# Kernel tuning notes

Measured on AMD Instinct MI355X. Metric: run time of the kernel, lower is better.

Reference implementation:

```python
import jax, jax.numpy as jnp
import numpy as np

D_MODEL = 1024
D_HEAD = 64
RANK = 8
LEAF = 4
NUM_LEAVES = D_HEAD // LEAF            # 16
NUM_LEVELS = 4                          # log2(64/4)
BLOCK_SIZES = [4, 8, 16, 32]
RANKS = [min(RANK, b) for b in BLOCK_SIZES]   # [4,8,8,8]
NUM_NODES = [NUM_LEAVES // 2 ** (l + 1) for l in range(NUM_LEVELS)]  # [8,4,2,1]


def _elu1(x):
    return jax.nn.elu(x) + 1.0


def setup_inputs() -> dict:
    key = jax.random.key(0)
    ks = jax.random.split(key, 32)
    B, T = 8, 2048
    x = jax.random.normal(ks[0], (B, T, D_MODEL), jnp.float32)
    s_in = 1.0 / np.sqrt(D_MODEL)
    s_out = 1.0 / np.sqrt(D_HEAD)
    inp = {
        'x': x,
        'Wq': jax.random.normal(ks[1], (D_MODEL, D_HEAD), jnp.float32) * s_in,
        'Wk': jax.random.normal(ks[2], (D_MODEL, D_HEAD), jnp.float32) * s_in,
        'Wv': jax.random.normal(ks[3], (D_MODEL, D_HEAD), jnp.float32) * s_in,
        'Wo': jax.random.normal(ks[4], (D_HEAD, D_MODEL), jnp.float32) * s_out,
    }
    # Fixed orthonormal bases per level (torch.linalg.qr of randn in original)
    idx = 5
    for name in ['UL', 'VR', 'UR', 'VL']:
        for l in range(NUM_LEVELS):
            bs, rl = BLOCK_SIZES[l], RANKS[l]
            Q, _ = jnp.linalg.qr(jax.random.normal(ks[idx], (bs, rl), jnp.float32))
            inp[f'{name}{l}'] = Q
            idx += 1
    return inp


def _hss_forward(x, Wq, Wk, Wv, Wo, UL, VR, UR, VL):
    B, T, _ = x.shape
    q = _elu1(x @ Wq)   # (B,T,Dh)
    k = _elu1(x @ Wk)
    v = x @ Wv

    leaf0 = jnp.zeros((B, NUM_LEAVES, LEAF, LEAF), x.dtype)
    Ws0 = tuple(jnp.zeros((B, NUM_NODES[l], RANKS[l], RANKS[l]), x.dtype)
                for l in range(NUM_LEVELS))
    z0 = jnp.zeros((B, D_HEAD), x.dtype)

    def step(carry, kvq):
        leaf, Ws, z = carry
        k_t, v_t, q_t = kvq  # each (B, Dh)
        # rank-1 update: leaf diagonal blocks
        leaf = leaf + jnp.einsum('bni,bnj->bnij',
                                 k_t.reshape(B, NUM_LEAVES, LEAF),
                                 v_t.reshape(B, NUM_LEAVES, LEAF))
        newWs = []
        for l in range(NUM_LEVELS):
            bs, nn = BLOCK_SIZES[l], NUM_NODES[l]
            u_r = k_t.reshape(B, nn, 2 * bs)
            v_r = v_t.reshape(B, nn, 2 * bs)
            uL = jnp.einsum('bnd,dr->bnr', u_r[:, :, :bs], UL[l])
            vR = jnp.einsum('bnd,dr->bnr', v_r[:, :, bs:], VR[l])
            newWs.append(Ws[l] + jnp.einsum('bni,bnj->bnij', uL, vR))
        Ws = tuple(newWs)
        z = z + k_t
        # HSS matvec: y = S @ q_t
        y = jnp.einsum('bnij,bnj->bni', leaf,
                       q_t.reshape(B, NUM_LEAVES, LEAF)).reshape(B, D_HEAD)
        for l in range(NUM_LEVELS):
            bs, nn = BLOCK_SIZES[l], NUM_NODES[l]
            x_r = q_t.reshape(B, nn, 2 * bs)
            vr_x = jnp.einsum('bnd,dr->bnr', x_r[:, :, bs:], VR[l])
            y_top = jnp.einsum('dr,bnr->bnd', UL[l],
                               jnp.einsum('bnij,bnj->bni', Ws[l], vr_x))
            vl_x = jnp.einsum('bnd,dr->bnr', x_r[:, :, :bs], VL[l])
            y_bot = jnp.einsum('dr,bnr->bnd', UR[l],
                               jnp.einsum('bnji,bnj->bni', Ws[l], vl_x))
            y = y + jnp.concatenate([y_top, y_bot], axis=-1).reshape(B, D_HEAD)
        denom = jnp.maximum(jnp.sum(z * q_t, axis=-1, keepdims=True), 1e-6)
        return (leaf, Ws, z), y / denom

    kvq = (jnp.swapaxes(k, 0, 1), jnp.swapaxes(v, 0, 1), jnp.swapaxes(q, 0, 1))
    _, outs = jax.lax.scan(step, (leaf0, Ws0, z0), kvq)  # (T,B,Dh)
    out = jnp.swapaxes(outs, 0, 1)  # (B,T,Dh); dropout is identity in eval
    return out @ Wo


def reference(x, Wq, Wk, Wv, Wo,
              UL0, UL1, UL2, UL3,
              VR0, VR1, VR2, VR3,
              UR0, UR1, UR2, UR3,
              VL0, VL1, VL2, VL3):
    UL = (UL0, UL1, UL2, UL3)
    VR = (VR0, VR1, VR2, VR3)
    UR = (UR0, UR1, UR2, UR3)
    VL = (VL0, VL1, VL2, VL3)
    return _hss_forward(x, Wq, Wk, Wv, Wo, UL, VR, UR, VL)
```

## Files before the change

### kernel.cpp

```cpp
#include <hip/hip_runtime.h>
#include <hip/hip_bf16.h>

typedef unsigned short u16;
typedef __attribute__((ext_vector_type(8))) short bf16x8;
typedef __attribute__((ext_vector_type(4))) float f32x4;

#define B_ 8
#define T_ 2048
#define BT_ (B_*T_)
#define DM_ 1024
#define DH_ 64
#define NCH_ 128
#define S_ (T_/NCH_)
#define STATE_ 896
#define UVP 180

__device__ __forceinline__ float b2f(u16 u){ unsigned v=((unsigned)u)<<16; float f; __builtin_memcpy(&f,&v,4); return f; }
__device__ __forceinline__ u16 f2b(float f){ __hip_bfloat16 h=__float2bfloat16(f); u16 u; __builtin_memcpy(&u,&h,2); return u; }

__device__ __forceinline__ float ldin(const void* p, size_t i, int f32){
  return f32 ? ((const float*)p)[i] : b2f(((const u16*)p)[i]);
}
__device__ __forceinline__ bf16x8 ld8bf(const void* p, size_t i, int f32){
  if (f32){
    f32x4 v0 = *(const f32x4*)((const float*)p + i);
    f32x4 v1 = *(const f32x4*)((const float*)p + i + 4);
    bf16x8 r;
    #pragma unroll
    for (int j=0;j<4;j++){ r[j] = (short)f2b(v0[j]); r[4+j] = (short)f2b(v1[j]); }
    return r;
  }
  return *(const bf16x8*)((const u16*)p + i);
}

__device__ __forceinline__ void gl_lds16(const void* g, void* l){
  __builtin_amdgcn_global_load_lds((const __attribute__((address_space(1))) unsigned int*)g,
                                   (__attribute__((address_space(3))) unsigned int*)l, 16, 0, 0);
}

__device__ __forceinline__ void decodeWs(int e, int& ia, int& ib){
  if (e<384){ int o=e-256, n=o>>4; ia=n*4+((o>>2)&3); ib=n*4+(o&3); }
  else if (e<640){ int o=e-384, n=o>>6; ia=32+n*8+((o>>3)&7); ib=32+n*8+(o&7); }
  else if (e<768){ int o=e-640, n=o>>6; ia=64+n*8+((o>>3)&7); ib=64+n*8+(o&7); }
  else { int o=e-768; ia=80+((o>>3)&7); ib=80+(o&7); }
}
__device__ __forceinline__ void decode88(int f, int& l, int& n, int& ri){
  if (f<32){ l=0; n=f>>2; ri=f&3; }
  else if (f<64){ l=1; n=(f-32)>>3; ri=f&7; }
  else if (f<80){ l=2; n=(f-64)>>3; ri=f&7; }
  else { l=3; n=0; ri=f&7; }
}

__global__ __launch_bounds__(64) void k_detect(const u16* __restrict__ x, int* __restrict__ flag){
  int tid = threadIdx.x;
  int sane = 0;
  for (int i = tid; i < 4096; i += 64){
    u16 u = x[i];
    int e = (u >> 7) & 0xFF;
    if ((u & 0x7FFF) == 0 || (e >= 100 && e <= 140)) sane++;
  }
  #pragma unroll
  for (int o = 32; o > 0; o >>= 1) sane += __shfl_down(sane, o);
  if (tid == 0) flag[0] = (sane < 3600) ? 1 : 0;
}

__global__ __launch_bounds__(256) void k_wfrag(
    const void* __restrict__ Wq, const void* __restrict__ Wk, const void* __restrict__ Wv,
    const void* __restrict__ Wo,
    const void* __restrict__ UL0, const void* __restrict__ UL1, const void* __restrict__ UL2, const void* __restrict__ UL3,
    const void* __restrict__ VR0, const void* __restrict__ VR1, const void* __restrict__ VR2, const void* __restrict__ VR3,
    const void* __restrict__ VL0, const void* __restrict__ VL1, const void* __restrict__ VL2, const void* __restrict__ VL3,
    u16* __restrict__ WF, u16* __restrict__ WoF, u16* __restrict__ PF,
    const int* __restrict__ fl)
{
  const int f32 = fl[0];
  int e = blockIdx.x*256 + threadIdx.x;
  if (e < 24576){
    int m = e >> 13;
    int rem = e & 8191;
    int ks = rem >> 8;
    int nt = (rem >> 6) & 3;
    int lane = rem & 63;
    const void* W = (m==0)?Wq:((m==1)?Wk:Wv);
    int kr = ks*32 + (lane>>4)*8;
    int col = nt*16 + (lane&15);
    u16 o[8];
    #pragma unroll
    for (int j=0;j<8;j++) o[j] = f2b(ldin(W, (size_t)(kr+j)*DH_ + col, f32));
    u16* dst = WF + (size_t)e*8;
    #pragma unroll
    for (int j=0;j<8;j++) dst[j] = o[j];
  } else if (e < 32768){
    int eo = e - 24576;
    int ks = eo >> 12;
    int nt = (eo >> 6) & 63;
    int lane = eo & 63;
    int kr = ks*32 + (lane>>4)*8;
    int col = nt*16 + (lane&15);
    u16 o[8];
    #pragma unroll
    for (int j=0;j<8;j++) o[j] = f2b(ldin(Wo, (size_t)(kr+j)*DM_ + col, f32));
    u16* dst = WoF + (size_t)eo*8;
    #pragma unroll
    for (int j=0;j<8;j++) dst[j] = o[j];
  } else if (e < 35072){
    int pe = e - 32768;
    int lane = pe & 63;
    int nt = (pe >> 6) % 6;
    int mk = pe / 384;
    int ks = mk & 1, mat = mk >> 1;
    int col = nt*16 + (lane&15);
    int dbase = ks*32 + (lane>>4)*8;
    const int BSl[4]={4,8,16,32}; const int Rl[4]={4,8,8,8};
    u16 o[8];
    #pragma unroll
    for (int j=0;j<8;j++){
      float val = 0.f;
      if (col < 88){
        int l,n,ri; decode88(col,l,n,ri);
        int bs=BSl[l], r=Rl[l];
        int lo = n*2*bs + ((mat==1)?bs:0);
        int d = dbase + j;
        if (d >= lo && d < lo+bs){
          const void* Up;
          if (mat==0)      Up = (l==0)?UL0:(l==1)?UL1:(l==2)?UL2:UL3;
          else if (mat==1) Up = (l==0)?VR0:(l==1)?VR1:(l==2)?VR2:VR3;
          else             Up = (l==0)?VL0:(l==1)?VL1:(l==2)?VL2:VL3;
          val = ldin(Up, (size_t)(d-lo)*r + ri, f32);
        }
      }
      o[j] = f2b(val);
    }
    u16* dst = PF + (size_t)pe*8;
    #pragma unroll
    for (int j=0;j<8;j++) dst[j] = o[j];
  }
}

__global__ __launch_bounds__(512, 4) void k_proj7(
    const void* __restrict__ x, const u16* __restrict__ WF,
    float* __restrict__ oq, float* __restrict__ ok_, float* __restrict__ ov,
    u16* __restrict__ qb16, u16* __restrict__ kb16, u16* __restrict__ vb16,
    const int* __restrict__ fl)
{
  __shared__ __align__(16) char sh[49152];
  const int f32 = fl[0];
  const int tid = threadIdx.x;
  const int wv = tid>>6;
  const int mg = wv>>1;
  const int h  = wv&1;
  const int lane = tid&63;
  const int quad = lane>>4, l16 = lane&15;
  const int rows0 = blockIdx.x*64 + mg*16;
  const size_t rowA = (size_t)(rows0 + l16)*DM_;

  f32x4 acc[12];
  #pragma unroll
  for (int i=0;i<12;i++) acc[i] = (f32x4){0.f,0.f,0.f,0.f};

  #define STAGE(t, buf) do{                                                   \
    _Pragma("unroll")                                                         \
    for (int r=0;r<3;r++){                                                    \
      int s = wv + r*8;                                                       \
      int hs = (s>=12) ? 1 : 0;                                               \
      int f = s - hs*12;                                                      \
      int m_ = f>>2, nt_ = f&3;                                               \
      int ks_ = hs*16 + (t);                                                  \
      const char* src = (const char*)WF + (size_t)((m_*32+ks_)*4+nt_)*1024 + (size_t)lane*16; \
      char* dst = sh + (buf)*24576 + hs*12288 + f*1024 + lane*16;             \
      gl_lds16(src, dst);                                                     \
    } }while(0)

  STAGE(0, 0);
  bf16x8 a_cur = ld8bf(x, rowA + (size_t)(h*16)*32 + quad*8, f32);
  asm volatile("s_waitcnt vmcnt(0)" ::: "memory");
  __syncthreads();

  bf16x8 a_nxt = a_cur;
  for (int t=0;t<16;t++){
    int buf = t&1;
    if (t<15){
      STAGE(t+1, buf^1);
      a_nxt = ld8bf(x, rowA + (size_t)(h*16+t+1)*32 + quad*8, f32);
    }
    const char* bb = sh + buf*24576 + h*12288;
    #pragma unroll
    for (int f=0;f<12;f++){
      bf16x8 b = *(const bf16x8*)(bb + f*1024 + lane*16);
      acc[f] = __builtin_amdgcn_mfma_f32_16x16x32_bf16(a_cur, b, acc[f],0,0,0);
    }
    a_cur = a_nxt;
    asm volatile("s_waitcnt vmcnt(0)" ::: "memory");
    __syncthreads();
  }
  #undef STAGE

  if (h==1){
    #pragma unroll
    for (int i=0;i<12;i++) ((f32x4*)sh)[(mg*12+i)*64 + lane] = acc[i];
  }
  __syncthreads();
  if (h==0){
    #pragma unroll
    for (int i=0;i<12;i++){
      f32x4 r = ((f32x4*)sh)[(mg*12+i)*64 + lane];
      acc[i][0]+=r[0]; acc[i][1]+=r[1]; acc[i][2]+=r[2]; acc[i][3]+=r[3];
    }
    #pragma unroll
    for (int m=0;m<3;m++){
      float* __restrict__ outp = (m==0)?oq:((m==1)?ok_:ov);
      u16* __restrict__ outb = (m==0)?qb16:((m==1)?kb16:vb16);
      #pragma unroll
      for (int nt=0;nt<4;nt++){
        #pragma unroll
        for (int i=0;i<4;i++){
          int row = rows0 + quad*4 + i;
          int col = nt*16 + l16;
          float val = acc[m*4+nt][i];
          if (m<2) val = (val>0.f)? (val+1.f) : expf(val);
          outp[(size_t)row*DH_ + col] = val;
          outb[(size_t)row*DH_ + col] = f2b(val);
        }
      }
    }
  }
}

__global__ __launch_bounds__(64) void k_prep3(
    const u16* __restrict__ qb16, const u16* __restrict__ kb16, const u16* __restrict__ vb16,
    const u16* __restrict__ PF,
    float* __restrict__ uLa, float* __restrict__ vRa, float* __restrict__ vrxa, float* __restrict__ vlxa)
{
  const int m = blockIdx.y;
  const int rows0 = blockIdx.x*16;
  const int lane = threadIdx.x;
  const int quad = lane>>4, l16 = lane&15;

  const u16* __restrict__ src = (m==0)?kb16:((m==1)?vb16:qb16);
  const int mat = (m==0)?0:((m==3)?2:1);

  bf16x8 a[2];
  #pragma unroll
  for (int ks=0;ks<2;ks++){
    size_t off = (size_t)(rows0 + l16)*DH_ + ks*32 + quad*8;
    a[ks] = *(const bf16x8*)(src + off);
  }
  f32x4 acc[6];
  #pragma unroll
  for (int nt=0;nt<6;nt++) acc[nt] = (f32x4){0.f,0.f,0.f,0.f};

  #pragma unroll
  for (int ks=0;ks<2;ks++){
    #pragma unroll
    for (int nt=0;nt<6;nt++){
      bf16x8 b = *(const bf16x8*)(PF + ((size_t)((mat*2+ks)*6+nt)*64 + lane)*8);
      acc[nt] = __builtin_amdgcn_mfma_f32_16x16x32_bf16(a[ks], b, acc[nt],0,0,0);
    }
  }
  float* __restrict__ dst = (m==0)?uLa:(m==1)?vRa:(m==2)?vrxa:vlxa;
  #pragma unroll
  for (int nt=0;nt<6;nt++){
    int col = nt*16 + l16;
    if (col < 88){
      #pragma unroll
      for (int i=0;i<4;i++){
        int row = rows0 + quad*4 + i;
        dst[(size_t)row*88 + col] = acc[nt][i];
      }
    }
  }
}

__global__ __launch_bounds__(256) void k_chunksum(
    const float* __restrict__ gk, const float* __restrict__ gv,
    const float* __restrict__ uLa, const float* __restrict__ vRa,
    float* __restrict__ SL)
{
  const int bid = blockIdx.x;
  const int b = bid/NCH_, c = bid%NCH_;
  const size_t base64 = (size_t)(b*T_ + c*S_)*64;
  const size_t base88 = (size_t)(b*T_ + c*S_)*88;
  for (int p=0;p<4;p++){
    int e = threadIdx.x + p*256;
    if (e>=STATE_) break;
    float acc=0.f;
    if (e < 256){
      int n=e>>4;
      const float* A = gk + base64 + n*4 + ((e>>2)&3);
      const float* Bp = gv + base64 + n*4 + (e&3);
      for (int s=0;s<S_;s++) acc += A[s*64]*Bp[s*64];
    } else if (e < 832){
      int ia, ib; decodeWs(e, ia, ib);
      const float* A = uLa + base88 + ia;
      const float* Bp = vRa + base88 + ib;
      for (int s=0;s<S_;s++) acc += A[s*88]*Bp[s*88];
    } else {
      const float* A = gk + base64 + (e-832);
      for (int s=0;s<S_;s++) acc += A[s*64];
    }
    SL[(size_t)bid*STATE_ + e] = acc;
  }
}

__global__ __launch_bounds__(224) void k_prefix(const float* __restrict__ SL, float* __restrict__ SP){
  const int b = blockIdx.x;
  int e = blockIdx.y*224 + threadIdx.x;
  if (e >= STATE_) return;
  float run=0.f;
  for (int c=0;c<NCH_;c++){
    size_t idx = ((size_t)(b*NCH_+c))*STATE_ + e;
    SP[idx] = run; run += SL[idx];
  }
}

__global__ __launch_bounds__(128) void k_intra(
    const float* __restrict__ gq, const float* __restrict__ gk, const float* __restrict__ gv,
    const float* __restrict__ uLa, const float* __restrict__ vRa,
    const float* __restrict__ vrxa, const float* __restrict__ vlxa,
    const float* __restrict__ SP,
    const void* __restrict__ UL0, const void* __restrict__ UL1, const void* __restrict__ UL2, const void* __restrict__ UL3,
    const void* __restrict__ UR0, const void* __restrict__ UR1, const void* __restrict__ UR2, const void* __restrict__ UR3,
    u16* __restrict__ Yb, const int* __restrict__ fl)
{
  __shared__ float kS[S_*64];
  __shared__ float vS[S_*64];
  __shared__ float uvS[S_*UVP];
  __shared__ float st0[STATE_];
  __shared__ float ULs[520], URs[520];
  const int f32 = fl[0];
  const int tid = threadIdx.x;
  const int bid = blockIdx.x;
  const int b = bid/NCH_, c = bid%NCH_;
  const int row0 = b*T_ + c*S_;

  const size_t r64 = (size_t)row0*64;
  for (int i=tid;i<S_*64;i+=128){ kS[i]=gk[r64+i]; vS[i]=gv[r64+i]; }
  const size_t r88 = (size_t)row0*88;
  for (int i=tid;i<S_*88;i+=128){
    int s=i/88, f=i-s*88;
    uvS[s*UVP+f]    = uLa[r88+i];
    uvS[s*UVP+88+f] = vRa[r88+i];
  }
  for (int e=tid;e<STATE_;e+=128) st0[e] = SP[(size_t)bid*STATE_+e];
  for (int e=tid;e<464;e+=128){
    int l, idx;
    if (e<16){ l=0; idx=e; } else if (e<80){ l=1; idx=e-16; }
    else if (e<208){ l=2; idx=e-80; } else { l=3; idx=e-208; }
    const void* ul = (l==0)?UL0:(l==1)?UL1:(l==2)?UL2:UL3;
    const void* ur = (l==0)?UR0:(l==1)?UR1:(l==2)?UR2:UR3;
    int dst = (l==0) ? e :
              (l==1) ? 16  + (idx>>3)*9 + (idx&7) :
              (l==2) ? 88  + (idx>>3)*9 + (idx&7) :
                       232 + (idx>>3)*9 + (idx&7);
    ULs[dst] = ldin(ul, idx, f32); URs[dst] = ldin(ur, idx, f32);
  }
  __syncthreads();

  const int w = tid>>6, lane = tid&63, tl = lane>>3, g = lane&7;
  const int t = w*8 + tl;
  const int n1 = g>>1, ri1 = (g&1)*4;
  const int n2 = g>>2, ri2 = (g&3)*2;
  const size_t row = (size_t)(row0 + t);

  float qr[8];
  { const float* qp = gq + row*64 + g*8;
    *(f32x4*)&qr[0] = *(const f32x4*)qp; *(f32x4*)&qr[4] = *(const f32x4*)(qp+4); }
  float rxL0[4], lxL0[4], rxL1[8], lxL1[8], rxL2[8], lxL2[8], rxL3[8], lxL3[8];
  { const float* rp = vrxa + row*88; const float* lp = vlxa + row*88;
    *(f32x4*)&rxL0[0] = *(const f32x4*)(rp + 4*g);
    *(f32x4*)&lxL0[0] = *(const f32x4*)(lp + 4*g);
    *(f32x4*)&rxL1[0] = *(const f32x4*)(rp + 32 + n1*8); *(f32x4*)&rxL1[4] = *(const f32x4*)(rp + 36 + n1*8);
    *(f32x4*)&lxL1[0] = *(const f32x4*)(lp + 32 + n1*8); *(f32x4*)&lxL1[4] = *(const f32x4*)(lp + 36 + n1*8);
    *(f32x4*)&rxL2[0] = *(const f32x4*)(rp + 64 + n2*8); *(f32x4*)&rxL2[4] = *(const f32x4*)(rp + 68 + n2*8);
    *(f32x4*)&lxL2[0] = *(const f32x4*)(lp + 64 + n2*8); *(f32x4*)&lxL2[4] = *(const f32x4*)(lp + 68 + n2*8);
    *(f32x4*)&rxL3[0] = *(const f32x4*)(rp + 80); *(f32x4*)&rxL3[4] = *(const f32x4*)(rp + 84);
    *(f32x4*)&lxL3[0] = *(const f32x4*)(lp + 80); *(f32x4*)&lxL3[4] = *(const f32x4*)(lp + 84); }

  float yacc[8], den = 0.f;
  #pragma unroll
  for (int cc=0;cc<8;cc++){
    int n = 2*g + (cc>>2);
    const float* m = &st0[n*16 + (cc&3)*4];
    const float* qp = &qr[(cc>>2)*4];
    yacc[cc] = m[0]*qp[0]+m[1]*qp[1]+m[2]*qp[2]+m[3]*qp[3];
    den += st0[832 + g*8 + cc]*qr[cc];
  }
  float gtL0[4], gbL0[4], gtL1[4], gbL1[4], gtL2[2], gbL2[2], gtL3, gbL3;
  #pragma unroll
  for (int cc=0;cc<4;cc++){
    const float* m = &st0[256 + g*16 + cc*4];
    gtL0[cc] = m[0]*rxL0[0]+m[1]*rxL0[1]+m[2]*rxL0[2]+m[3]*rxL0[3];
    float s2 = 0.f;
    #pragma unroll
    for (int j=0;j<4;j++) s2 += st0[256 + g*16 + j*4 + cc]*lxL0[j];
    gbL0[cc] = s2;
  }
  #pragma unroll
  for (int cc=0;cc<4;cc++){
    int ri = ri1 + cc;
    float s1=0.f, s2=0.f;
    #pragma unroll
    for (int j=0;j<8;j++){
      s1 += st0[384 + n1*64 + ri*8 + j]*rxL1[j];
      s2 += st0[384 + n1*64 + j*8 + ri]*lxL1[j];
    }
    gtL1[cc]=s1; gbL1[cc]=s2;
  }
  #pragma unroll
  for (int cc=0;cc<2;cc++){
    int ri = ri2 + cc;
    float s1=0.f, s2=0.f;
    #pragma unroll
    for (int j=0;j<8;j++){
      s1 += st0[640 + n2*64 + ri*8 + j]*rxL2[j];
      s2 += st0[640 + n2*64 + j*8 + ri]*lxL2[j];
    }
    gtL2[cc]=s1; gbL2[cc]=s2;
  }
  { float s1=0.f, s2=0.f;
    #pragma unroll
    for (int j=0;j<8;j++){
      s1 += st0[768 + g*8 + j]*rxL3[j];
      s2 += st0[768 + j*8 + g]*lxL3[j];
    }
    gtL3=s1; gbL3=s2; }

  const int smax = w*8 + 8;
  for (int s=0; s<smax; s++){
    const float* ks_ = &kS[s*64 + g*8];
    const float* vs_ = &vS[s*64 + g*8];
    const float* uL_ = &uvS[s*UVP];
    const float* vR_ = &uvS[s*UVP + 88];
    float dv0 = vs_[0]*qr[0]+vs_[1]*qr[1]+vs_[2]*qr[2]+vs_[3]*qr[3];
    float dv1 = vs_[4]*qr[4]+vs_[5]*qr[5]+vs_[6]*qr[6]+vs_[7]*qr[7];
    float dn = 0.f;
    #pragma unroll
    for (int cc=0;cc<8;cc++) dn += ks_[cc]*qr[cc];
    float d1L0=0.f,d2L0=0.f;
    #pragma unroll
    for (int j=0;j<4;j++){ d1L0 += vR_[4*g+j]*rxL0[j]; d2L0 += uL_[4*g+j]*lxL0[j]; }
    float d1L1=0.f,d2L1=0.f;
    #pragma unroll
    for (int j=0;j<8;j++){ d1L1 += vR_[32+n1*8+j]*rxL1[j]; d2L1 += uL_[32+n1*8+j]*lxL1[j]; }
    float d1L2=0.f,d2L2=0.f;
    #pragma unroll
    for (int j=0;j<8;j++){ d1L2 += vR_[64+n2*8+j]*rxL2[j]; d2L2 += uL_[64+n2*8+j]*lxL2[j]; }
    float d1L3=0.f,d2L3=0.f;
    #pragma unroll
    for (int j=0;j<8;j++){ d1L3 += vR_[80+j]*rxL3[j]; d2L3 += uL_[80+j]*lxL3[j]; }
    if (s<=t){
      den += dn;
      #pragma unroll
      for (int cc=0;cc<8;cc++) yacc[cc] += ks_[cc]*((cc<4)?dv0:dv1);
      #pragma unroll
      for (int cc=0;cc<4;cc++){
        gtL0[cc] += uL_[4*g+cc]*d1L0;          gbL0[cc] += vR_[4*g+cc]*d2L0;
        gtL1[cc] += uL_[32+n1*8+ri1+cc]*d1L1;  gbL1[cc] += vR_[32+n1*8+ri1+cc]*d2L1;
      }
      #pragma unroll
      for (int cc=0;cc<2;cc++){
        gtL2[cc] += uL_[64+n2*8+ri2+cc]*d1L2;  gbL2[cc] += vR_[64+n2*8+ri2+cc]*d2L2;
      }
      gtL3 += uL_[80+g]*d1L3;  gbL3 += vR_[80+g]*d2L3;
    }
  }
  __syncthreads();

  { float* gr = &uvS[t*UVP];
    #pragma unroll
    for (int cc=0;cc<4;cc++){
      gr[4*g+cc] = gtL0[cc];                 gr[88+4*g+cc] = gbL0[cc];
      gr[32+n1*8+ri1+cc] = gtL1[cc];         gr[88+32+n1*8+ri1+cc] = gbL1[cc];
    }
    #pragma unroll
    for (int cc=0;cc<2;cc++){
      gr[64+n2*8+ri2+cc] = gtL2[cc];         gr[88+64+n2*8+ri2+cc] = gbL2[cc];
    }
    gr[80+g] = gtL3;  gr[88+80+g] = gbL3;
  }
  __syncthreads();

  den += __shfl_xor(den,1); den += __shfl_xor(den,2); den += __shfl_xor(den,4);
  float inv = 1.f / fmaxf(den, 1e-6f);
  const float* gr = &uvS[t*UVP];
  float yout[8];
  #pragma unroll
  for (int cc=0;cc<8;cc++){
    int j = g*8 + cc;
    float y = yacc[cc];
    if (cc<4){
      #pragma unroll
      for (int rr=0;rr<4;rr++) y += ULs[cc*4+rr]*gr[g*4+rr];
    } else {
      #pragma unroll
      for (int rr=0;rr<4;rr++) y += URs[(cc-4)*4+rr]*gr[88+g*4+rr];
    }
    { int seg=j>>4, pos=j&15;
      if (pos<8){
        #pragma unroll
        for (int rr=0;rr<8;rr++) y += ULs[16+pos*9+rr]*gr[32+seg*8+rr];
      } else {
        #pragma unroll
        for (int rr=0;rr<8;rr++) y += URs[16+(pos-8)*9+rr]*gr[88+32+seg*8+rr];
      } }
    { int seg=j>>5, pos=j&31;
      if (pos<16){
        #pragma unroll
        for (int rr=0;rr<8;rr++) y += ULs[88+pos*9+rr]*gr[64+seg*8+rr];
      } else {
        #pragma unroll
        for (int rr=0;rr<8;rr++) y += URs[88+(pos-16)*9+rr]*gr[88+64+seg*8+rr];
      } }
    { int pos=j;
      if (pos<32){
        #pragma unroll
        for (int rr=0;rr<8;rr++) y += ULs[232+pos*9+rr]*gr[80+rr];
      } else {
        #pragma unroll
        for (int rr=0;rr<8;rr++) y += URs[232+(pos-32)*9+rr]*gr[88+80+rr];
      } }
    yout[cc] = y*inv;
  }
  u16* yp = Yb + row*64 + g*8;
  ushort4 o1, o2;
  o1.x=f2b(yout[0]); o1.y=f2b(yout[1]); o1.z=f2b(yout[2]); o1.w=f2b(yout[3]);
  o2.x=f2b(yout[4]); o2.y=f2b(yout[5]); o2.z=f2b(yout[6]); o2.w=f2b(yout[7]);
  *(ushort4*)yp = o1;
  *(ushort4*)(yp+4) = o2;
}

__global__ __launch_bounds__(64,4) void k_outproj3(
    const u16* __restrict__ Yb, const u16* __restrict__ WoF, void* __restrict__ outv,
    const int* __restrict__ fl)
{
  const int f32 = fl[0];
  const int rows0 = blockIdx.x*32;
  const int nt0 = blockIdx.y*8;
  const int lane = threadIdx.x;
  const int quad = lane>>4, l16 = lane&15;

  f32x4 acc[16];
  #pragma unroll
  for (int i=0;i<16;i++) acc[i] = (f32x4){0.f,0.f,0.f,0.f};

  #pragma unroll
  for (int ks=0;ks<2;ks++){
    int ko = ks*32 + quad*8;
    bf16x8 a0 = *(const bf16x8*)(Yb + (size_t)(rows0 + l16)*DH_ + ko);
    bf16x8 a1 = *(const bf16x8*)(Yb + (size_t)(rows0 + 16 + l16)*DH_ + ko);
    #pragma unroll
    for (int nt=0;nt<8;nt++){
      bf16x8 b = *(const bf16x8*)(WoF + ((size_t)(ks*64 + nt0 + nt)*64 + lane)*8);
      acc[nt]   = __builtin_amdgcn_mfma_f32_16x16x32_bf16(a0,b,acc[nt],0,0,0);
      acc[8+nt] = __builtin_amdgcn_mfma_f32_16x16x32_bf16(a1,b,acc[8+nt],0,0,0);
    }
  }
  #pragma unroll
  for (int sp=0;sp<2;sp++){
    #pragma unroll
    for (int nt=0;nt<8;nt++){
      #pragma unroll
      for (int i=0;i<4;i++){
        int row = rows0 + sp*16 + quad*4 + i;
        int col = (nt0+nt)*16 + l16;
        size_t idx = (size_t)row*DM_ + col;
        float v = acc[sp*8+nt][i];
        if (f32) ((float*)outv)[idx] = v;
        else ((u16*)outv)[idx] = f2b(v);
      }
    }
  }
}

extern "C" void kernel_launch(void* const* d_in, const int* in_sizes, int n_in,
                              void* d_out, int out_size, void* d_ws, size_t ws_size,
                              hipStream_t stream) {
  const void* x  = d_in[0];
  const void* Wq = d_in[1];
  const void* Wk = d_in[2];
  const void* Wv = d_in[3];
  const void* Wo = d_in[4];
  const void* UL[4] = {d_in[5],d_in[6],d_in[7],d_in[8]};
  const void* VR[4] = {d_in[9],d_in[10],d_in[11],d_in[12]};
  const void* UR[4] = {d_in[13],d_in[14],d_in[15],d_in[16]};
  const void* VL[4] = {d_in[17],d_in[18],d_in[19],d_in[20]};

  int* flag = (int*)d_ws;
  float* ws = (float*)d_ws + 16;
  float* q    = ws;
  float* kf   = q    + (size_t)BT_*64;
  float* vf   = kf   + (size_t)BT_*64;
  float* uLa  = vf   + (size_t)BT_*64;
  float* vRa  = uLa  + (size_t)BT_*88;
  float* vrxa = vRa  + (size_t)BT_*88;
  float* vlxa = vrxa + (size_t)BT_*88;
  float* SL   = vlxa + (size_t)BT_*88;
  float* SP   = SL   + (size_t)B_*NCH_*STATE_;
  u16*   Yb   = (u16*)(SP + (size_t)B_*NCH_*STATE_);
  u16*   WF   = Yb  + (size_t)BT_*64;
  u16*   WoF  = WF  + (size_t)196608;
  u16*   PF   = WoF + (size_t)65536;
  u16*   qb16 = PF  + (size_t)18432;
  u16*   kb16 = qb16 + (size_t)BT_*64;
  u16*   vb16 = kb16 + (size_t)BT_*64;

  k_detect<<<1, 64, 0, stream>>>((const u16*)x, flag);
  k_wfrag<<<137, 256, 0, stream>>>(Wq, Wk, Wv, Wo,
      UL[0],UL[1],UL[2],UL[3], VR[0],VR[1],VR[2],VR[3], VL[0],VL[1],VL[2],VL[3],
      WF, WoF, PF, flag);
  k_proj7<<<BT_/64, 512, 0, stream>>>(x, WF, q, kf, vf, qb16, kb16, vb16, flag);
  k_prep3<<<dim3(BT_/16, 4), 64, 0, stream>>>(qb16, kb16, vb16, PF, uLa, vRa, vrxa, vlxa);
  k_chunksum<<<B_*NCH_, 256, 0, stream>>>(kf, vf, uLa, vRa, SL);
  k_prefix<<<dim3(B_, 4), 224, 0, stream>>>(SL, SP);
  k_intra<<<B_*NCH_, 128, 0, stream>>>(q, kf, vf, uLa, vRa, vrxa, vlxa, SP,
      UL[0],UL[1],UL[2],UL[3], UR[0],UR[1],UR[2],UR[3], Yb, flag);
  k_outproj3<<<dim3(512, 8), 64, 0, stream>>>(Yb, WoF, d_out, flag);
}
```

Before: 242.3 us.

## Triple-buffer weight staging and preload all x fragments in projection kernel

```diff
diff --git a/kernel.cpp b/kernel.cpp
--- a/kernel.cpp
+++ b/kernel.cpp
@@ -137,13 +137,13 @@
   }
 }
 
-__global__ __launch_bounds__(512, 4) void k_proj7(
+__global__ __launch_bounds__(512, 1) void k_proj8(
     const void* __restrict__ x, const u16* __restrict__ WF,
     float* __restrict__ oq, float* __restrict__ ok_, float* __restrict__ ov,
     u16* __restrict__ qb16, u16* __restrict__ kb16, u16* __restrict__ vb16,
     const int* __restrict__ fl)
 {
-  __shared__ __align__(16) char sh[49152];
+  __shared__ __align__(16) char sh[73728];
   const int f32 = fl[0];
   const int tid = threadIdx.x;
   const int wv = tid>>6;
@@ -171,29 +171,30 @@
       gl_lds16(src, dst);                                                     \
     } }while(0)
 
+  bf16x8 a[16];
+  #pragma unroll
+  for (int t=0;t<16;t++) a[t] = ld8bf(x, rowA + (size_t)(h*16+t)*32 + quad*8, f32);
   STAGE(0, 0);
-  bf16x8 a_cur = ld8bf(x, rowA + (size_t)(h*16)*32 + quad*8, f32);
-  asm volatile("s_waitcnt vmcnt(0)" ::: "memory");
-  __syncthreads();
-
-  bf16x8 a_nxt = a_cur;
+  STAGE(1, 1);
+  __builtin_amdgcn_sched_barrier(0);
+
+  #pragma unroll
   for (int t=0;t<16;t++){
-    int buf = t&1;
-    if (t<15){
-      STAGE(t+1, buf^1);
-      a_nxt = ld8bf(x, rowA + (size_t)(h*16+t+1)*32 + quad*8, f32);
-    }
-    const char* bb = sh + buf*24576 + h*12288;
+    if (t<15) asm volatile("s_waitcnt vmcnt(3)" ::: "memory");
+    else      asm volatile("s_waitcnt vmcnt(0)" ::: "memory");
+    __builtin_amdgcn_s_barrier();
+    __builtin_amdgcn_sched_barrier(0);
+    const char* bb = sh + (t%3)*24576 + h*12288;
     #pragma unroll
     for (int f=0;f<12;f++){
       bf16x8 b = *(const bf16x8*)(bb + f*1024 + lane*16);
-      acc[f] = __builtin_amdgcn_mfma_f32_16x16x32_bf16(a_cur, b, acc[f],0,0,0);
-    }
-    a_cur = a_nxt;
-    asm volatile("s_waitcnt vmcnt(0)" ::: "memory");
-    __syncthreads();
+      acc[f] = __builtin_amdgcn_mfma_f32_16x16x32_bf16(a[t], b, acc[f],0,0,0);
+    }
+    if (t<14) STAGE(t+2, (t+2)%3);
+    __builtin_amdgcn_sched_barrier(0);
   }
   #undef STAGE
+  __syncthreads();
 
   if (h==1){
     #pragma unroll
@@ -608,7 +609,7 @@
   k_wfrag<<<137, 256, 0, stream>>>(Wq, Wk, Wv, Wo,
       UL[0],UL[1],UL[2],UL[3], VR[0],VR[1],VR[2],VR[3], VL[0],VL[1],VL[2],VL[3],
       WF, WoF, PF, flag);
-  k_proj7<<<BT_/64, 512, 0, stream>>>(x, WF, q, kf, vf, qb16, kb16, vb16, flag);
+  k_proj8<<<BT_/64, 512, 0, stream>>>(x, WF, q, kf, vf, qb16, kb16, vb16, flag);
   k_prep3<<<dim3(BT_/16, 4), 64, 0, stream>>>(qb16, kb16, vb16, PF, uLa, vRa, vrxa, vlxa);
   k_chunksum<<<B_*NCH_, 256, 0, stream>>>(kf, vf, uLa, vRa, SL);
   k_prefix<<<dim3(B_, 4), 224, 0, stream>>>(SL, SP);
```

New measurement: 241.9 us. About the same (-0.2%).
